# Kernel optimization log

Hardware: AMD Instinct MI355X
Metric: run time of the kernel (lower is better)

Reference implementation:

```python
import jax, jax.numpy as jnp
import numpy as np

D = 768        # embed_dim
H = 12         # num_heads
DEPTH = 12
P = 16         # patch size
IMG = 224
G = IMG // P   # 14 patches per side
NPATCH = G * G # 196
N = NPATCH + 1 # seq len with cls token
MLP = 4 * D    # 3072
NC = 1000      # num_classes
EPS = 1e-6


def _ln(x, w, b):
    m = jnp.mean(x, axis=-1, keepdims=True)
    v = jnp.mean((x - m) ** 2, axis=-1, keepdims=True)
    return (x - m) / jnp.sqrt(v + EPS) * w + b


def setup_inputs() -> dict:
    key = jax.random.key(0)
    ks = jax.random.split(key, 12)
    f = lambda k, s: jax.random.normal(k, s, jnp.float32) * 0.02
    return {
        "x": jax.random.normal(ks[0], (32, 3, IMG, IMG), jnp.float32),
        "patch_w": f(ks[1], (3 * P * P, D)),  # Conv2d(3,768,16,16) as matmul
        "patch_b": jnp.zeros((D,), jnp.float32),
        "cls_token": f(ks[2], (1, 1, D)),
        "pos_embed": f(ks[3], (1, N, D)),
        "ln1_w": jnp.ones((DEPTH, D), jnp.float32),
        "ln1_b": jnp.zeros((DEPTH, D), jnp.float32),
        "qkv_w": f(ks[4], (DEPTH, D, 3 * D)),
        "qkv_b": jnp.zeros((DEPTH, 3 * D), jnp.float32),
        "proj_w": f(ks[5], (DEPTH, D, D)),
        "proj_b": jnp.zeros((DEPTH, D), jnp.float32),
        "ln2_w": jnp.ones((DEPTH, D), jnp.float32),
        "ln2_b": jnp.zeros((DEPTH, D), jnp.float32),
        "fc1_w": f(ks[6], (DEPTH, D, MLP)),
        "fc1_b": jnp.zeros((DEPTH, MLP), jnp.float32),
        "fc2_w": f(ks[7], (DEPTH, MLP, D)),
        "fc2_b": jnp.zeros((DEPTH, D), jnp.float32),
        "normf_w": jnp.ones((D,), jnp.float32),
        "normf_b": jnp.zeros((D,), jnp.float32),
        "head_w": f(ks[8], (D, NC)),
        "head_b": jnp.zeros((NC,), jnp.float32),
    }


def _fwd(x, patch_w, patch_b, cls_token, pos_embed, ln1_w, ln1_b, qkv_w, qkv_b,
         proj_w, proj_b, ln2_w, ln2_b, fc1_w, fc1_b, fc2_w, fc2_b,
         normf_w, normf_b, head_w, head_b):
    B = x.shape[0]
    # Patch embed: equivalent to Conv2d(3, D, kernel=16, stride=16)
    patches = x.reshape(B, 3, G, P, G, P).transpose(0, 2, 4, 1, 3, 5)
    patches = patches.reshape(B, NPATCH, 3 * P * P)
    h = patches @ patch_w + patch_b                       # [B, 196, D]
    cls = jnp.broadcast_to(cls_token, (B, 1, D))
    h = jnp.concatenate([cls, h], axis=1) + pos_embed     # [B, N, D]
    scale = (D // H) ** -0.5

    def block(h, p):
        l1w, l1b, qw, qb, pw, pb, l2w, l2b, f1w, f1b, f2w, f2b = p
        y = _ln(h, l1w, l1b)
        qkv = (y @ qw + qb).reshape(B, N, 3, H, D // H).transpose(2, 0, 3, 1, 4)
        q, k, v = qkv[0], qkv[1], qkv[2]                  # [B, H, N, dh]
        attn = jax.nn.softmax(jnp.einsum('bhnd,bhmd->bhnm', q, k) * scale, axis=-1)
        o = jnp.einsum('bhnm,bhmd->bhnd', attn, v).transpose(0, 2, 1, 3).reshape(B, N, D)
        h = h + (o @ pw + pb)
        y = _ln(h, l2w, l2b)
        h = h + (jax.nn.gelu(y @ f1w + f1b, approximate=False) @ f2w + f2b)
        return h, None

    params = (ln1_w, ln1_b, qkv_w, qkv_b, proj_w, proj_b,
              ln2_w, ln2_b, fc1_w, fc1_b, fc2_w, fc2_b)
    h, _ = jax.lax.scan(block, h, params)
    h = _ln(h, normf_w, normf_b)
    return h[:, 0] @ head_w + head_b                      # [B, 1000]


def reference(x, patch_w, patch_b, cls_token, pos_embed, ln1_w, ln1_b, qkv_w, qkv_b,
              proj_w, proj_b, ln2_w, ln2_b, fc1_w, fc1_b, fc2_w, fc2_b,
              normf_w, normf_b, head_w, head_b):
    return _fwd(x, patch_w, patch_b, cls_token, pos_embed, ln1_w, ln1_b, qkv_w, qkv_b,
                proj_w, proj_b, ln2_w, ln2_b, fc1_w, fc1_b, fc2_w, fc2_b,
                normf_w, normf_b, head_w, head_b)
```

## Files before the change

kernel.cpp:

```cpp
#include <hip/hip_runtime.h>
#include <hip/hip_bf16.h>
#include <type_traits>


#define BV   32
#define DIM  768
#define NHD  12
#define DH   64
#define NSEQ 197
#define NPAT 196
#define MLPD 3072
#define NCLS 1000
#define NLAYER 12

typedef __hip_bfloat16 bf16;
typedef __attribute__((ext_vector_type(8))) short s8v;
typedef __attribute__((ext_vector_type(4))) float f32x4;

#define GLDS16(gp, lp) __builtin_amdgcn_global_load_lds( \
    (const __attribute__((address_space(1))) void*)(gp), \
    (__attribute__((address_space(3))) void*)(lp), 16, 0, 0)

__device__ __forceinline__ short f2bf(float v) {
    return (short)__bfloat16_as_ushort(__float2bfloat16(v));
}

template<int ACT, bool RESID, typename TO, int MI>
__global__ __launch_bounds__(256)
void bgemm(const bf16* __restrict__ A, const bf16* __restrict__ B,
           const float* __restrict__ bias, TO* __restrict__ C,
           int M, int N, int K, int lda, int ldb, int ldc)
{
    constexpr int BM    = MI * 32;
    constexpr int ASIZE = MI * 1024;
    constexpr int BUFS  = ASIZE + 4096;
    __shared__ short As[3 * BUFS];

    int nbx = gridDim.x;
    int nb  = nbx * gridDim.y;
    int bid = blockIdx.y * nbx + blockIdx.x;
    {
        int per = nb >> 3, rem = nb & 7;
        int x = bid & 7, loc = bid >> 3;
        bid = x * per + (x < rem ? x : rem) + loc;
    }
    const int m0 = (bid / nbx) * BM;
    const int n0 = (bid % nbx) * 128;

    const int tid  = threadIdx.x;
    const int wave = tid >> 6;
    const int lane = tid & 63;

    const int c0 = wave * 2, c1 = c0 + 1;
    const int rsub = lane >> 2;
    const int kp8  = (((lane & 3) ^ ((rsub >> 1) & 3)) * 8);

    int ra0, ra1;
    if constexpr (MI == 4) { ra0 = m0 + c0 * 16 + rsub; ra1 = m0 + c1 * 16 + rsub; }
    else                   { ra0 = m0 + wave * 16 + rsub; ra1 = ra0; }
    if (ra0 > M - 1) ra0 = M - 1;
    if (ra1 > M - 1) ra1 = M - 1;
    int rb0 = n0 + c0 * 16 + rsub; if (rb0 > N - 1) rb0 = N - 1;
    int rb1 = n0 + c1 * 16 + rsub; if (rb1 > N - 1) rb1 = N - 1;

    const bf16* pa0 = A + (long)ra0 * lda + kp8;
    const bf16* pa1 = A + (long)ra1 * lda + kp8;
    const bf16* pb0 = B + (long)rb0 * ldb + kp8;
    const bf16* pb1 = B + (long)rb1 * ldb + kp8;

    const int wm = wave >> 1, wn = wave & 1;
    const int colr = lane & 15;
    const int quad = lane >> 4;

    f32x4 acc[MI][4];
    #pragma unroll
    for (int i = 0; i < MI; ++i)
        #pragma unroll
        for (int j = 0; j < 4; ++j)
            acc[i][j] = (f32x4){0.f, 0.f, 0.f, 0.f};

    const int sq = quad ^ ((colr >> 1) & 3);
    const short* AsP = &As[(wm * (MI * 16) + colr) * 32 + sq * 8];
    const short* BsP = &As[ASIZE + (wn * 64 + colr) * 32 + sq * 8];

    auto STAGE = [&](int bufi) {
        int _o = bufi * BUFS;
        if constexpr (MI == 4) {
            GLDS16(pa0, &As[_o + c0 * 512]);
            GLDS16(pa1, &As[_o + c1 * 512]);
            pa1 += 32;
        } else {
            GLDS16(pa0, &As[_o + wave * 512]);
        }
        GLDS16(pb0, &As[_o + ASIZE + c0 * 512]);
        GLDS16(pb1, &As[_o + ASIZE + c1 * 512]);
        pa0 += 32; pb0 += 32; pb1 += 32;
    };

    const int nt = K >> 5;
    STAGE(0);
    STAGE(1);
    int cur = 0, nxt = 2;

    for (int t = 0; t < nt; ++t) {
        if (t + 2 < nt) {
            STAGE(nxt);
            nxt = (nxt == 2) ? 0 : nxt + 1;
            if constexpr (MI == 4) asm volatile("s_waitcnt vmcnt(8)" ::: "memory");
            else                   asm volatile("s_waitcnt vmcnt(6)" ::: "memory");
        } else if (t + 1 < nt) {
            if constexpr (MI == 4) asm volatile("s_waitcnt vmcnt(4)" ::: "memory");
            else                   asm volatile("s_waitcnt vmcnt(3)" ::: "memory");
        } else {
            asm volatile("s_waitcnt vmcnt(0)" ::: "memory");
        }
        __builtin_amdgcn_s_barrier();
        asm volatile("" ::: "memory");

        const short* Ab = AsP + cur * BUFS;
        const short* Bb = BsP + cur * BUFS;
        s8v a[MI], b[4];
        #pragma unroll
        for (int i = 0; i < MI; ++i) a[i] = *(const s8v*)(Ab + i * 512);
        #pragma unroll
        for (int j = 0; j < 4; ++j) b[j] = *(const s8v*)(Bb + j * 512);
        #pragma unroll
        for (int i = 0; i < MI; ++i)
            #pragma unroll
            for (int j = 0; j < 4; ++j)
                acc[i][j] = __builtin_amdgcn_mfma_f32_16x16x32_bf16(
                    a[i], b[j], acc[i][j], 0, 0, 0);

        cur = (cur == 2) ? 0 : cur + 1;
        asm volatile("" ::: "memory");
        __builtin_amdgcn_s_barrier();
        asm volatile("" ::: "memory");
    }

    float* ep = ((float*)As) + wave * 1024;
    const int lrow = lane >> 2;
    const int lc4  = (lane & 3) * 16;

    #pragma unroll
    for (int i = 0; i < MI; ++i) {
        #pragma unroll
        for (int j = 0; j < 4; ++j)
            #pragma unroll
            for (int r = 0; r < 4; ++r)
                ep[(quad * 4 + r) * 64 + j * 16 + colr] = acc[i][j][r];
        __syncthreads();

        int gm = m0 + wm * (MI * 16) + i * 16 + lrow;
        int gn = n0 + wn * 64 + lc4;
        if (gm < M) {
            float vals[16];
            #pragma unroll
            for (int c = 0; c < 16; ++c) vals[c] = ep[lrow * 64 + lc4 + c];

            if (gn + 16 <= N) {
                if (bias) {
                    #pragma unroll
                    for (int c = 0; c < 16; ++c) vals[c] += bias[gn + c];
                }
                if (ACT == 1) {
                    #pragma unroll
                    for (int c = 0; c < 16; ++c)
                        vals[c] = 0.5f * vals[c] *
                                  (1.0f + erff(vals[c] * 0.70710678118654752f));
                }
                if constexpr (std::is_same<TO, float>::value) {
                    float* Cp = (float*)C + (long)gm * ldc + gn;
                    if constexpr (RESID) {
                        #pragma unroll
                        for (int c4 = 0; c4 < 4; ++c4) {
                            f32x4 old = *(const f32x4*)&Cp[c4 * 4];
                            #pragma unroll
                            for (int e = 0; e < 4; ++e) vals[c4 * 4 + e] += old[e];
                        }
                    }
                    #pragma unroll
                    for (int c4 = 0; c4 < 4; ++c4) {
                        f32x4 v;
                        #pragma unroll
                        for (int e = 0; e < 4; ++e) v[e] = vals[c4 * 4 + e];
                        *(f32x4*)&Cp[c4 * 4] = v;
                    }
                } else {
                    short* Cp = (short*)C + (long)gm * ldc + gn;
                    s8v v0, v1;
                    #pragma unroll
                    for (int e = 0; e < 8; ++e) { v0[e] = f2bf(vals[e]); v1[e] = f2bf(vals[8 + e]); }
                    *(s8v*)&Cp[0] = v0;
                    *(s8v*)&Cp[8] = v1;
                }
            } else {
                #pragma unroll
                for (int c = 0; c < 16; ++c) {
                    int g = gn + c;
                    if (g >= N) continue;
                    float v = vals[c];
                    if (bias) v += bias[g];
                    if (ACT == 1) v = 0.5f * v * (1.0f + erff(v * 0.70710678118654752f));
                    long idx = (long)gm * ldc + g;
                    if constexpr (RESID) v += ((const float*)C)[idx];
                    if constexpr (std::is_same<TO, float>::value) C[idx] = v;
                    else C[idx] = __float2bfloat16(v);
                }
            }
        }
        __syncthreads();
    }
}

__global__ __launch_bounds__(256)
void attn_kernel(const bf16* __restrict__ qkv, bf16* __restrict__ O)
{
    __shared__ short Ks[14848];
    __shared__ short Vt[14848];

    const int tid  = threadIdx.x;
    const int wave = tid >> 6;
    const int lane = tid & 63;
    const int q0 = blockIdx.x * 64;
    const int b  = blockIdx.y / NHD;
    const int h  = blockIdx.y % NHD;
    const bf16* base = qkv + (long)b * NSEQ * (3 * DIM);

    const int colr = lane & 15;
    const int quad = lane >> 4;

    int qr = q0 + wave * 16 + colr; if (qr > NSEQ - 1) qr = NSEQ - 1;
    const bf16* qp = &base[(long)qr * (3 * DIM) + h * DH + quad * 8];
    s8v qa0 = *(const s8v*)qp;
    s8v qa1 = *(const s8v*)(qp + 32);

    const int seqL = tid & 31, dc = tid >> 5;
    s8v vreg[7];
    #pragma unroll
    for (int st = 0; st < 7; ++st) {
        int gr = st * 32 + seqL; if (gr > NSEQ - 1) gr = NSEQ - 1;
        vreg[st] = *(const s8v*)&base[(long)gr * (3 * DIM) + 2 * DIM + h * DH + dc * 8];
    }

    {
        int r8   = lane >> 3;
        int scol = ((lane & 7) ^ r8) * 8;
        #pragma unroll
        for (int p = 0; p < 7; ++p) {
            int chunk = wave * 7 + p;
            int gr = chunk * 8 + r8; if (gr > NSEQ - 1) gr = NSEQ - 1;
            GLDS16(&base[(long)gr * (3 * DIM) + DIM + h * DH + scol],
                   &Ks[chunk * 512]);
        }
    }

    #pragma unroll
    for (int st = 0; st < 7; ++st) {
        int seq = st * 32 + seqL;
        #pragma unroll
        for (int i = 0; i < 8; ++i)
            Vt[(dc * 8 + i) * 232 + seq] = vreg[st][i];
    }
    __syncthreads();

    f32x4 s[14];
    #pragma unroll
    for (int j = 0; j < 14; ++j) s[j] = (f32x4){0.f, 0.f, 0.f, 0.f};
    #pragma unroll
    for (int j = 0; j < 14; ++j) {
        int rb = (j * 16 + colr) * 64;
        s8v bf0 = *(const s8v*)&Ks[rb + ((quad ^ (colr & 7)) * 8)];
        s[j] = __builtin_amdgcn_mfma_f32_16x16x32_bf16(qa0, bf0, s[j], 0, 0, 0);
        s8v bf1 = *(const s8v*)&Ks[rb + (((quad + 4) ^ (colr & 7)) * 8)];
        s[j] = __builtin_amdgcn_mfma_f32_16x16x32_bf16(qa1, bf1, s[j], 0, 0, 0);
    }

    float mx[4] = {-1e30f, -1e30f, -1e30f, -1e30f};
    #pragma unroll
    for (int j = 0; j < 14; ++j) {
        int c = j * 16 + colr;
        #pragma unroll
        for (int r = 0; r < 4; ++r) {
            s[j][r] *= 0.125f;
            if (c < NSEQ) mx[r] = fmaxf(mx[r], s[j][r]);
        }
    }
    #pragma unroll
    for (int off = 1; off <= 8; off <<= 1)
        #pragma unroll
        for (int r = 0; r < 4; ++r)
            mx[r] = fmaxf(mx[r], __shfl_xor(mx[r], off));

    float sum[4] = {0.f, 0.f, 0.f, 0.f};
    #pragma unroll
    for (int j = 0; j < 14; ++j) {
        int c = j * 16 + colr;
        #pragma unroll
        for (int r = 0; r < 4; ++r) {
            float v = (c < NSEQ) ? expf(s[j][r] - mx[r]) : 0.f;
            s[j][r] = v;
            sum[r] += v;
        }
    }
    #pragma unroll
    for (int off = 1; off <= 8; off <<= 1)
        #pragma unroll
        for (int r = 0; r < 4; ++r)
            sum[r] += __shfl_xor(sum[r], off);
    float inv[4];
    #pragma unroll
    for (int r = 0; r < 4; ++r) inv[r] = 1.0f / sum[r];

    __syncthreads();
    short* P = Ks;
    #pragma unroll
    for (int j = 0; j < 14; ++j)
        #pragma unroll
        for (int r = 0; r < 4; ++r)
            P[(wave * 16 + quad * 4 + r) * 232 + j * 16 + colr] =
                f2bf(s[j][r] * inv[r]);

    __syncthreads();

    f32x4 o[4];
    #pragma unroll
    for (int j2 = 0; j2 < 4; ++j2) o[j2] = (f32x4){0.f, 0.f, 0.f, 0.f};
    #pragma unroll
    for (int ks = 0; ks < 7; ++ks) {
        s8v a = *(const s8v*)&P[(wave * 16 + colr) * 232 + quad * 8 + ks * 32];
        #pragma unroll
        for (int j2 = 0; j2 < 4; ++j2) {
            s8v bf = *(const s8v*)&Vt[(j2 * 16 + colr) * 232 + quad * 8 + ks * 32];
            o[j2] = __builtin_amdgcn_mfma_f32_16x16x32_bf16(a, bf, o[j2], 0, 0, 0);
        }
    }

    #pragma unroll
    for (int j2 = 0; j2 < 4; ++j2)
        #pragma unroll
        for (int r = 0; r < 4; ++r) {
            int qrow = q0 + wave * 16 + quad * 4 + r;
            if (qrow < NSEQ)
                O[((long)b * NSEQ + qrow) * DIM + h * DH + j2 * 16 + colr] =
                    __float2bfloat16(o[j2][r]);
        }
}

__device__ __forceinline__ void wconv_tile(const float* __restrict__ in,
                                           bf16* __restrict__ out,
                                           int R, int C, int bx, int by)
{
    __shared__ float t[32][33];
    int c0 = bx * 32, r0 = by * 32;
    int tx = threadIdx.x & 31, ty = threadIdx.x >> 5;
    #pragma unroll
    for (int i = 0; i < 4; ++i) {
        int r = r0 + ty + 8 * i;
        if (r < R && c0 + tx < C) t[ty + 8 * i][tx] = in[(long)r * C + c0 + tx];
    }
    __syncthreads();
    #pragma unroll
    for (int i = 0; i < 4; ++i) {
        int c = c0 + ty + 8 * i;
        int r = r0 + tx;
        if (c < C && r < R) out[(long)c * R + r] = __float2bfloat16(t[tx][ty + 8 * i]);
    }
}

__global__ __launch_bounds__(256)
void wconv_kernel(const float* __restrict__ in, bf16* __restrict__ out,
                  int R, int C)
{
    wconv_tile(in, out, R, C, blockIdx.x, blockIdx.y);
}

__global__ __launch_bounds__(256)
void wconv4_kernel(const float* __restrict__ qw, const float* __restrict__ pw,
                   const float* __restrict__ f1w, const float* __restrict__ f2w,
                   bf16* __restrict__ qT, bf16* __restrict__ pT,
                   bf16* __restrict__ f1T, bf16* __restrict__ f2T)
{
    int bid = blockIdx.x;
    if (bid < 1728)      { int t = bid;        wconv_tile(qw,  qT,  768,  2304, t % 72, t / 72); }
    else if (bid < 2304) { int t = bid - 1728; wconv_tile(pw,  pT,  768,  768,  t % 24, t / 24); }
    else if (bid < 4608) { int t = bid - 2304; wconv_tile(f1w, f1T, 768,  3072, t % 96, t / 96); }
    else                 { int t = bid - 4608; wconv_tile(f2w, f2T, 3072, 768,  t % 24, t / 24); }
}

__global__ __launch_bounds__(256)
void ln_kernel(const float* __restrict__ in, long in_stride,
               bf16* __restrict__ out, long out_stride,
               const float* __restrict__ w, const float* __restrict__ b,
               int nrows)
{
    int wave = threadIdx.x >> 6, lane = threadIdx.x & 63;
    long r = (long)blockIdx.x * 4 + wave;
    if (r >= nrows) return;
    const float* x = in + r * in_stride;
    bf16* y = out + r * out_stride;

    f32x4 c[3];
    float s = 0.f, s2 = 0.f;
    #pragma unroll
    for (int p = 0; p < 3; ++p) {
        c[p] = *(const f32x4*)&x[p * 256 + lane * 4];
        #pragma unroll
        for (int e = 0; e < 4; ++e) { s += c[p][e]; s2 += c[p][e] * c[p][e]; }
    }
    #pragma unroll
    for (int off = 1; off <= 32; off <<= 1) {
        s  += __shfl_xor(s, off);
        s2 += __shfl_xor(s2, off);
    }
    float mean = s * (1.0f / (float)DIM);
    float var  = s2 * (1.0f / (float)DIM) - mean * mean;
    float rstd = 1.0f / sqrtf(var + 1e-6f);

    #pragma unroll
    for (int p = 0; p < 3; ++p) {
        f32x4 wv = *(const f32x4*)&w[p * 256 + lane * 4];
        f32x4 bv = *(const f32x4*)&b[p * 256 + lane * 4];
        #pragma unroll
        for (int e = 0; e < 4; ++e)
            y[p * 256 + lane * 4 + e] =
                __float2bfloat16((c[p][e] - mean) * rstd * wv[e] + bv[e]);
    }
}

__global__ __launch_bounds__(256)
void im2col_kernel(const float* __restrict__ x, bf16* __restrict__ out)
{
    long i = (long)blockIdx.x * 256 + threadIdx.x;
    const long total = (long)BV * NPAT * DIM;
    if (i >= total) return;
    int col = (int)(i % DIM);
    long row = i / DIM;
    int c  = col >> 8;
    int py = (col >> 4) & 15;
    int px = col & 15;
    int b  = (int)(row / NPAT);
    int pp = (int)(row % NPAT);
    int gy = pp / 14, gx = pp % 14;
    out[i] = __float2bfloat16(
        x[(((long)(b * 3 + c) * 224 + gy * 16 + py) * 224) + gx * 16 + px]);
}

__global__ __launch_bounds__(256)
void assemble_kernel(const float* __restrict__ tmp, const float* __restrict__ cls,
                     const float* __restrict__ pos, float* __restrict__ h)
{
    long i = (long)blockIdx.x * 256 + threadIdx.x;
    const long total = (long)BV * NSEQ * DIM;
    if (i >= total) return;
    int d = (int)(i % DIM);
    long row = i / DIM;
    int n = (int)(row % NSEQ);
    long b = row / NSEQ;
    float v;
    if (n == 0) v = cls[d];
    else        v = tmp[(b * NPAT + (n - 1)) * DIM + d];
    h[i] = v + pos[(long)n * DIM + d];
}

extern "C" void kernel_launch(void* const* d_in, const int* in_sizes, int n_in,
                              void* d_out, int out_size, void* d_ws, size_t ws_size,
                              hipStream_t stream)
{
    const float* x        = (const float*)d_in[0];
    const float* patch_w  = (const float*)d_in[1];
    const float* patch_b  = (const float*)d_in[2];
    const float* cls_tok  = (const float*)d_in[3];
    const float* pos_emb  = (const float*)d_in[4];
    const float* ln1_w    = (const float*)d_in[5];
    const float* ln1_b    = (const float*)d_in[6];
    const float* qkv_w    = (const float*)d_in[7];
    const float* qkv_b    = (const float*)d_in[8];
    const float* proj_w   = (const float*)d_in[9];
    const float* proj_b   = (const float*)d_in[10];
    const float* ln2_w    = (const float*)d_in[11];
    const float* ln2_b    = (const float*)d_in[12];
    const float* fc1_w    = (const float*)d_in[13];
    const float* fc1_b    = (const float*)d_in[14];
    const float* fc2_w    = (const float*)d_in[15];
    const float* fc2_b    = (const float*)d_in[16];
    const float* normf_w  = (const float*)d_in[17];
    const float* normf_b  = (const float*)d_in[18];
    const float* head_w   = (const float*)d_in[19];
    const float* head_b   = (const float*)d_in[20];
    float* out = (float*)d_out;

    const long M = (long)BV * NSEQ;
    const long MP = (long)BV * NPAT;

    float* h      = (float*)d_ws;
    float* ptmp   = h + 4841472L;
    bf16*  qkv    = (bf16*)(ptmp + 4816896L);
    bf16*  lnout  = qkv + 14524416L;
    bf16*  big    = lnout + 4841472L;
    bf16*  wT     = big + 19365888L;
    bf16*  qkvT = wT;
    bf16*  projT = wT + 1769472L;
    bf16*  fc1T  = wT + 2359296L;
    bf16*  fc2T  = wT + 4718592L;

    dim3 blk(256);

    wconv_kernel<<<dim3(24, 24), blk, 0, stream>>>(patch_w, qkvT, DIM, DIM);
    im2col_kernel<<<dim3((unsigned)((MP * DIM + 255) / 256)), blk, 0, stream>>>(x, big);
    bgemm<0, false, float, 2><<<dim3(6, 98), blk, 0, stream>>>(
        big, qkvT, patch_b, ptmp, (int)MP, DIM, DIM, DIM, DIM, DIM);
    assemble_kernel<<<dim3((unsigned)((M * DIM + 255) / 256)), blk, 0, stream>>>(
        ptmp, cls_tok, pos_emb, h);

    for (int l = 0; l < NLAYER; ++l) {
        wconv4_kernel<<<dim3(6912), blk, 0, stream>>>(
            qkv_w + (long)l * DIM * 3 * DIM, proj_w + (long)l * DIM * DIM,
            fc1_w + (long)l * DIM * MLPD,    fc2_w + (long)l * MLPD * DIM,
            qkvT, projT, fc1T, fc2T);

        ln_kernel<<<dim3((unsigned)((M + 3) / 4)), blk, 0, stream>>>(
            h, DIM, lnout, DIM, ln1_w + (long)l * DIM, ln1_b + (long)l * DIM, (int)M);

        bgemm<0, false, bf16, 4><<<dim3(18, 50), blk, 0, stream>>>(
            lnout, qkvT, qkv_b + (long)l * 3 * DIM, qkv,
            (int)M, 3 * DIM, DIM, DIM, DIM, 3 * DIM);

        attn_kernel<<<dim3(4, BV * NHD), blk, 0, stream>>>(qkv, lnout);

        bgemm<0, true, float, 2><<<dim3(6, 99), blk, 0, stream>>>(
            lnout, projT, proj_b + (long)l * DIM, h,
            (int)M, DIM, DIM, DIM, DIM, DIM);

        ln_kernel<<<dim3((unsigned)((M + 3) / 4)), blk, 0, stream>>>(
            h, DIM, lnout, DIM, ln2_w + (long)l * DIM, ln2_b + (long)l * DIM, (int)M);

        bgemm<1, false, bf16, 4><<<dim3(24, 50), blk, 0, stream>>>(
            lnout, fc1T, fc1_b + (long)l * MLPD, big,
            (int)M, MLPD, DIM, DIM, DIM, MLPD);

        bgemm<0, true, float, 2><<<dim3(6, 99), blk, 0, stream>>>(
            big, fc2T, fc2_b + (long)l * DIM, h,
            (int)M, DIM, MLPD, MLPD, MLPD, DIM);
    }

    ln_kernel<<<dim3(8), blk, 0, stream>>>(
        h, (long)NSEQ * DIM, lnout, DIM, normf_w, normf_b, BV);

    wconv_kernel<<<dim3(32, 24), blk, 0, stream>>>(head_w, qkvT, DIM, NCLS);
    bgemm<0, false, float, 2><<<dim3(8, 1), blk, 0, stream>>>(
        lnout, qkvT, head_b, out, BV, NCLS, DIM, DIM, DIM, NCLS);
}
```

Baseline: 3.109 ms.

## Load GEMM A operand directly into registers, keep only B in LDS

The bf16 GEMM now loads the A tile straight from global memory into triple-buffered register fragments, in MFMA layout, instead of staging it through LDS. Only B still goes through LDS via global_load_lds. The main loop is unrolled by three to rotate the register buffers, and the vmcnt waits are adjusted for the extra loads. This cuts LDS footprint and LDS read traffic for A. In exchange, both waves that share a row block fetch the same A rows from global memory, register pressure goes up, and the loop assumes K/32 is a multiple of three.

```diff
diff --git a/kernel.cpp b/kernel.cpp
--- a/kernel.cpp
+++ b/kernel.cpp
@@ -31,10 +31,8 @@
            const float* __restrict__ bias, TO* __restrict__ C,
            int M, int N, int K, int lda, int ldb, int ldc)
 {
-    constexpr int BM    = MI * 32;
-    constexpr int ASIZE = MI * 1024;
-    constexpr int BUFS  = ASIZE + 4096;
-    __shared__ short As[3 * BUFS];
+    constexpr int BM = MI * 32;
+    __shared__ short Bs[3 * 4096];
 
     int nbx = gridDim.x;
     int nb  = nbx * gridDim.y;
@@ -55,16 +53,8 @@
     const int rsub = lane >> 2;
     const int kp8  = (((lane & 3) ^ ((rsub >> 1) & 3)) * 8);
 
-    int ra0, ra1;
-    if constexpr (MI == 4) { ra0 = m0 + c0 * 16 + rsub; ra1 = m0 + c1 * 16 + rsub; }
-    else                   { ra0 = m0 + wave * 16 + rsub; ra1 = ra0; }
-    if (ra0 > M - 1) ra0 = M - 1;
-    if (ra1 > M - 1) ra1 = M - 1;
     int rb0 = n0 + c0 * 16 + rsub; if (rb0 > N - 1) rb0 = N - 1;
     int rb1 = n0 + c1 * 16 + rsub; if (rb1 > N - 1) rb1 = N - 1;
-
-    const bf16* pa0 = A + (long)ra0 * lda + kp8;
-    const bf16* pa1 = A + (long)ra1 * lda + kp8;
     const bf16* pb0 = B + (long)rb0 * ldb + kp8;
     const bf16* pb1 = B + (long)rb1 * ldb + kp8;
 
@@ -72,6 +62,14 @@
     const int colr = lane & 15;
     const int quad = lane >> 4;
 
+    const bf16* pAf[MI];
+    #pragma unroll
+    for (int i = 0; i < MI; ++i) {
+        int rA = m0 + wm * (MI * 16) + i * 16 + colr;
+        if (rA > M - 1) rA = M - 1;
+        pAf[i] = A + (long)rA * lda + quad * 8;
+    }
+
     f32x4 acc[MI][4];
     #pragma unroll
     for (int i = 0; i < MI; ++i)
@@ -80,64 +78,69 @@
             acc[i][j] = (f32x4){0.f, 0.f, 0.f, 0.f};
 
     const int sq = quad ^ ((colr >> 1) & 3);
-    const short* AsP = &As[(wm * (MI * 16) + colr) * 32 + sq * 8];
-    const short* BsP = &As[ASIZE + (wn * 64 + colr) * 32 + sq * 8];
-
-    auto STAGE = [&](int bufi) {
-        int _o = bufi * BUFS;
-        if constexpr (MI == 4) {
-            GLDS16(pa0, &As[_o + c0 * 512]);
-            GLDS16(pa1, &As[_o + c1 * 512]);
-            pa1 += 32;
-        } else {
-            GLDS16(pa0, &As[_o + wave * 512]);
-        }
-        GLDS16(pb0, &As[_o + ASIZE + c0 * 512]);
-        GLDS16(pb1, &As[_o + ASIZE + c1 * 512]);
-        pa0 += 32; pb0 += 32; pb1 += 32;
-    };
+    const short* BsP = &Bs[(wn * 64 + colr) * 32 + sq * 8];
+
+#define BSTAGE(bufi) do {                               \
+        GLDS16(pb0, &Bs[(bufi) * 4096 + c0 * 512]);     \
+        GLDS16(pb1, &Bs[(bufi) * 4096 + c1 * 512]);     \
+        pb0 += 32; pb1 += 32;                           \
+    } while (0)
+
+#define ALOAD(AR, T) do {                               \
+        _Pragma("unroll")                               \
+        for (int i = 0; i < MI; ++i)                    \
+            AR[i] = *(const s8v*)(pAf[i] + (long)(T) * 32); \
+    } while (0)
 
     const int nt = K >> 5;
-    STAGE(0);
-    STAGE(1);
-    int cur = 0, nxt = 2;
-
-    for (int t = 0; t < nt; ++t) {
-        if (t + 2 < nt) {
-            STAGE(nxt);
-            nxt = (nxt == 2) ? 0 : nxt + 1;
-            if constexpr (MI == 4) asm volatile("s_waitcnt vmcnt(8)" ::: "memory");
-            else                   asm volatile("s_waitcnt vmcnt(6)" ::: "memory");
-        } else if (t + 1 < nt) {
-            if constexpr (MI == 4) asm volatile("s_waitcnt vmcnt(4)" ::: "memory");
-            else                   asm volatile("s_waitcnt vmcnt(3)" ::: "memory");
-        } else {
-            asm volatile("s_waitcnt vmcnt(0)" ::: "memory");
-        }
-        __builtin_amdgcn_s_barrier();
-        asm volatile("" ::: "memory");
-
-        const short* Ab = AsP + cur * BUFS;
-        const short* Bb = BsP + cur * BUFS;
-        s8v a[MI], b[4];
-        #pragma unroll
-        for (int i = 0; i < MI; ++i) a[i] = *(const s8v*)(Ab + i * 512);
-        #pragma unroll
-        for (int j = 0; j < 4; ++j) b[j] = *(const s8v*)(Bb + j * 512);
-        #pragma unroll
-        for (int i = 0; i < MI; ++i)
-            #pragma unroll
-            for (int j = 0; j < 4; ++j)
-                acc[i][j] = __builtin_amdgcn_mfma_f32_16x16x32_bf16(
-                    a[i], b[j], acc[i][j], 0, 0, 0);
-
-        cur = (cur == 2) ? 0 : cur + 1;
-        asm volatile("" ::: "memory");
-        __builtin_amdgcn_s_barrier();
-        asm volatile("" ::: "memory");
-    }
-
-    float* ep = ((float*)As) + wave * 1024;
+    s8v a0[MI], a1[MI], a2[MI];
+
+    BSTAGE(0); ALOAD(a0, 0);
+    BSTAGE(1); ALOAD(a1, 1);
+    BSTAGE(2); ALOAD(a2, 2);
+
+#define GBODY(T, BUF, AR) do {                                          \
+        if ((T) + 2 < nt) {                                             \
+            if constexpr (MI == 4)                                      \
+                asm volatile("s_waitcnt vmcnt(12)" ::: "memory");       \
+            else                                                        \
+                asm volatile("s_waitcnt vmcnt(8)" ::: "memory");        \
+        } else if ((T) + 1 < nt) {                                      \
+            if constexpr (MI == 4)                                      \
+                asm volatile("s_waitcnt vmcnt(6)" ::: "memory");        \
+            else                                                        \
+                asm volatile("s_waitcnt vmcnt(4)" ::: "memory");        \
+        } else {                                                        \
+            asm volatile("s_waitcnt vmcnt(0)" ::: "memory");            \
+        }                                                               \
+        __builtin_amdgcn_s_barrier();                                   \
+        asm volatile("" ::: "memory");                                  \
+        s8v b[4];                                                       \
+        _Pragma("unroll")                                               \
+        for (int j = 0; j < 4; ++j)                                     \
+            b[j] = *(const s8v*)(BsP + (BUF) * 4096 + j * 512);         \
+        _Pragma("unroll")                                               \
+        for (int i = 0; i < MI; ++i)                                    \
+            _Pragma("unroll")                                           \
+            for (int j = 0; j < 4; ++j)                                 \
+                acc[i][j] = __builtin_amdgcn_mfma_f32_16x16x32_bf16(    \
+                    AR[i], b[j], acc[i][j], 0, 0, 0);                   \
+        asm volatile("" ::: "memory");                                  \
+        __builtin_amdgcn_s_barrier();                                   \
+        asm volatile("" ::: "memory");                                  \
+        if ((T) + 3 < nt) { BSTAGE(BUF); ALOAD(AR, (T) + 3); }          \
+    } while (0)
+
+    for (int t = 0; t < nt; t += 3) {
+        GBODY(t + 0, 0, a0);
+        GBODY(t + 1, 1, a1);
+        GBODY(t + 2, 2, a2);
+    }
+#undef GBODY
+#undef ALOAD
+#undef BSTAGE
+
+    float* ep = ((float*)Bs) + wave * 1024;
     const int lrow = lane >> 2;
     const int lc4  = (lane & 3) * 16;
 
```

After: 4.331 ms. 39.3% more time.
